# Optimization experiments

Measured on AMD Instinct MI355X. Metric: run time of the kernel, lower is better.

Reference implementation:

```python
import jax, jax.numpy as jnp
import numpy as np

N, E = 50000, 800000
IN, HID, HEADS, LAT = 128, 64, 4, 32
NEG_SLOPE = 0.2  # PyG GATv2Conv default negative_slope


def _glorot(key, shape):
    fan_in, fan_out = shape[0], shape[-1]
    lim = (6.0 / (fan_in + fan_out)) ** 0.5
    return jax.random.uniform(key, shape, jnp.float32, -lim, lim)


def setup_inputs() -> dict:
    keys = jax.random.split(jax.random.key(0), 10)
    x = jax.random.normal(keys[0], (N, IN), jnp.float32)
    edge_index = jax.random.randint(keys[1], (2, E), 0, N, jnp.int32)
    return {
        "x": x,
        "edge_index": edge_index,
        # layer 1: in -> hidden, heads=HEADS, concat=True
        "W_l1": _glorot(keys[2], (IN, HEADS * HID)),
        "W_r1": _glorot(keys[3], (IN, HEADS * HID)),
        "att1": _glorot(keys[4], (HEADS, HID)),
        "bias1": jnp.zeros((HEADS * HID,), jnp.float32),
        # layer 2: heads*hidden -> latent, heads=1, concat=False
        "W_l2": _glorot(keys[5], (HEADS * HID, LAT)),
        "W_r2": _glorot(keys[6], (HEADS * HID, LAT)),
        "att2": _glorot(keys[7], (1, LAT)),
        "bias2": jnp.zeros((LAT,), jnp.float32),
    }


def gatv2_layer(x, src, dst, W_l, W_r, att, bias, heads, out_ch, concat):
    """PyG GATv2Conv (eval mode, add_self_loops already applied to src/dst)."""
    n = x.shape[0]
    xl = (x @ W_l).reshape(n, heads, out_ch)  # source transform (messages)
    xr = (x @ W_r).reshape(n, heads, out_ch)  # target transform
    # per-edge attention logits: a^T LeakyReLU(xl[j] + xr[i])
    e = jax.nn.leaky_relu(xl[src] + xr[dst], NEG_SLOPE)  # [E, H, C]
    score = jnp.einsum('ehc,hc->eh', e, att)             # [E, H]
    # segment softmax over incoming edges of each dst node
    smax = jax.ops.segment_max(score, dst, num_segments=n)   # [N, H]
    ex = jnp.exp(score - smax[dst])
    denom = jax.ops.segment_sum(ex, dst, num_segments=n)     # [N, H]
    alpha = ex / denom[dst]                                  # [E, H]
    # scatter-add weighted source features
    out = jax.ops.segment_sum(xl[src] * alpha[..., None], dst, num_segments=n)
    out = out.reshape(n, heads * out_ch) if concat else out.mean(axis=1)
    return out + bias


def reference(x, edge_index, W_l1, W_r1, att1, bias1, W_l2, W_r2, att2, bias2):
    n = x.shape[0]
    # GATv2Conv adds self loops by default
    loops = jnp.arange(n, dtype=edge_index.dtype)
    src = jnp.concatenate([edge_index[0], loops])
    dst = jnp.concatenate([edge_index[1], loops])
    h = jax.nn.elu(gatv2_layer(x, src, dst, W_l1, W_r1, att1, bias1, HEADS, HID, True))
    z = gatv2_layer(h, src, dst, W_l2, W_r2, att2, bias2, 1, LAT, False)
    # decode: sigmoid(<z[row], z[col]>) over the original edges
    row, col = edge_index[0], edge_index[1]
    pred = jax.nn.sigmoid(jnp.sum(z[row] * z[col], axis=1))
    return pred
```

## Files before the change

kernel.cpp:

```cpp
#include <hip/hip_runtime.h>
#include <hip/hip_fp16.h>
#include <math.h>

#define N_NODES 50000
#define N_EDGES 800000
#define EP (N_EDGES + N_NODES)
#define IN_CH 128
#define HID 64
#define HEADS 4
#define F1 (HEADS * HID)
#define LAT 32
#define NEG 0.2f
#define CAP 64
#define NW (512 * 128 + 64 * 256)
#define ZQ 412502

typedef __attribute__((ext_vector_type(8))) short short8;
typedef __attribute__((ext_vector_type(8))) unsigned short ushort8v;
typedef __attribute__((ext_vector_type(4))) float f32x4;
typedef __attribute__((ext_vector_type(4))) unsigned int uint4v;

__device__ __forceinline__ unsigned short f2bf(float f) {
    unsigned int x = __float_as_uint(f);
    x += 0x7fffu + ((x >> 16) & 1u);
    return (unsigned short)(x >> 16);
}
__device__ __forceinline__ float bf2f(unsigned short u) {
    return __uint_as_float(((unsigned int)u) << 16);
}
__device__ __forceinline__ float h2f(unsigned short u) {
    return __half2float(__ushort_as_half(u));
}
__device__ __forceinline__ f32x4 mfma_bf16(short8 a, short8 b, f32x4 c) {
    return __builtin_amdgcn_mfma_f32_16x16x32_bf16(a, b, c, 0, 0, 0);
}
__device__ __forceinline__ unsigned cvt_pk_bf16(float lo, float hi) {
    unsigned r;
    asm("v_cvt_pk_bf16_f32 %0, %1, %2" : "=v"(r) : "v"(lo), "v"(hi));
    return r;
}
__device__ __forceinline__ short8 pack_bf16x8(float4 A, float4 B) {
    uint4v u;
    u[0] = cvt_pk_bf16(A.x, A.y);
    u[1] = cvt_pk_bf16(A.z, A.w);
    u[2] = cvt_pk_bf16(B.x, B.y);
    u[3] = cvt_pk_bf16(B.z, B.w);
    return __builtin_bit_cast(short8, u);
}

__global__ void conv_w_zero(const float* __restrict__ Wl1, const float* __restrict__ Wr1,
                            const float* __restrict__ Wl2, const float* __restrict__ Wr2,
                            unsigned short* __restrict__ Wt1, unsigned short* __restrict__ Wt2,
                            int4* __restrict__ zbase) {
    int idx = blockIdx.x * 256 + threadIdx.x;
    if (idx < ZQ) zbase[idx] = make_int4(0, 0, 0, 0);
    if (idx < 512 * 128) {
        int n = idx >> 7, k = idx & 127;
        float v = (n < 256) ? Wl1[(size_t)k * 256 + n] : Wr1[(size_t)k * 256 + (n - 256)];
        Wt1[idx] = f2bf(v);
    } else if (idx < NW) {
        int j = idx - 512 * 128;
        int n = j >> 8, k = j & 255;
        float v = (n < 32) ? Wl2[(size_t)k * 32 + n] : Wr2[(size_t)k * 32 + (n - 32)];
        Wt2[j] = f2bf(v);
    }
}

__global__ __launch_bounds__(256) void gemm1_mfma(const float* __restrict__ x,
                                                  const unsigned short* __restrict__ Wt1,
                                                  unsigned short* __restrict__ xlh,
                                                  unsigned short* __restrict__ xrh) {
    int wave = threadIdx.x >> 6;
    int lane = threadIdx.x & 63;
    int quad = lane >> 4, lo = lane & 15;
    int row0 = blockIdx.x * 32;
    int colw = wave * 128;
    int rB0 = min(row0 + lo, N_NODES - 1);
    int rB1 = min(row0 + 16 + lo, N_NODES - 1);
    f32x4 acc[2][8];
#pragma unroll
    for (int rt = 0; rt < 2; rt++)
#pragma unroll
        for (int ct = 0; ct < 8; ct++) acc[rt][ct] = (f32x4){0.f, 0.f, 0.f, 0.f};
#pragma unroll
    for (int ks = 0; ks < 4; ks++) {
        int koff = ks * 32 + quad * 8;
        float4 fa0 = *(const float4*)(x + (size_t)rB0 * IN_CH + koff);
        float4 fb0 = *(const float4*)(x + (size_t)rB0 * IN_CH + koff + 4);
        float4 fa1 = *(const float4*)(x + (size_t)rB1 * IN_CH + koff);
        float4 fb1 = *(const float4*)(x + (size_t)rB1 * IN_CH + koff + 4);
        short8 b0 = pack_bf16x8(fa0, fb0);
        short8 b1 = pack_bf16x8(fa1, fb1);
#pragma unroll
        for (int ct = 0; ct < 8; ct++) {
            short8 a = *(const short8*)(Wt1 + (size_t)(colw + ct * 16 + lo) * IN_CH + koff);
            acc[0][ct] = mfma_bf16(a, b0, acc[0][ct]);
            acc[1][ct] = mfma_bf16(a, b1, acc[1][ct]);
        }
    }
#pragma unroll
    for (int rt = 0; rt < 2; rt++) {
        int node = row0 + rt * 16 + lo;
        if (node < N_NODES) {
#pragma unroll
            for (int ct = 0; ct < 8; ct++) {
                int feat = colw + ct * 16 + quad * 4;
                uint2 u;
                u.x = cvt_pk_bf16(acc[rt][ct][0], acc[rt][ct][1]);
                u.y = cvt_pk_bf16(acc[rt][ct][2], acc[rt][ct][3]);
                if (feat < F1)
                    *(uint2*)(xlh + (size_t)node * F1 + feat) = u;
                else
                    *(uint2*)(xrh + (size_t)node * F1 + (feat - F1)) = u;
            }
        }
    }
}

__global__ void scatter_bucket(const int* __restrict__ ei, int* __restrict__ cnt,
                               unsigned short* __restrict__ srcsP) {
    long e = (long)blockIdx.x * 256 + threadIdx.x;
    if (e >= EP) return;
    int s, d;
    if (e < N_EDGES) { s = ei[e]; d = ei[N_EDGES + e]; }
    else             { s = d = (int)(e - N_EDGES); }
    int pos = atomicAdd(&cnt[d], 1);
    if (pos < CAP) __builtin_nontemporal_store((unsigned short)s, &srcsP[(d << 6) + pos]);
}

__global__ __launch_bounds__(256) void fused_l1(const unsigned short* __restrict__ xlh,
                                                const unsigned short* __restrict__ xrh,
                                                unsigned short* __restrict__ hbf,
                                                const unsigned short* __restrict__ srcsP,
                                                const int* __restrict__ cnt,
                                                const float* __restrict__ att,
                                                const float* __restrict__ bias,
                                                int d0) {
    int wave = threadIdx.x >> 6;
    int lane = threadIdx.x & 63;
    int h = lane >> 5;
    int c = lane & 31;
    int c0 = c << 3;
    int d = d0 + blockIdx.x * 4 + wave;
    if (d >= N_NODES) return;
    ushort8v xru = *(const ushort8v*)(xrh + (size_t)d * F1 + c0);
    float4 atA = *(const float4*)(att + c0);
    float4 atB = *(const float4*)(att + c0 + 4);
    float xr8[8], at8[8] = {atA.x, atA.y, atA.z, atA.w, atB.x, atB.y, atB.z, atB.w};
    float a6[8], a4[8];
#pragma unroll
    for (int i = 0; i < 8; i++) {
        xr8[i] = bf2f(xru[i]);
        a6[i] = 0.6f * at8[i];
        a4[i] = 0.4f * at8[i];
    }
    int start = d << 6;
    int dg    = min(CAP, __builtin_amdgcn_readfirstlane(cnt[d]));
    float l = 0.f;
    float acc[8] = {};
    int jj = h;
    int s = srcsP[start + jj];
    ushort8v raw = *(const ushort8v*)(xlh + (size_t)s * F1 + c0);
    int sN = srcsP[start + jj + 2];
    int iters = (dg + 1) >> 1;
    for (int k = 0; k < iters; k++) {
        ushort8v cr = raw;
        raw = *(const ushort8v*)(xlh + (size_t)sN * F1 + c0);
        sN = srcsP[start + jj + 4];
        float a[8];
#pragma unroll
        for (int i = 0; i < 8; i++) a[i] = bf2f(cr[i]);
        float sc = 0.f;
#pragma unroll
        for (int i = 0; i < 8; i++) {
            float v = a[i] + xr8[i];
            sc = fmaf(v, a6[i], sc);
            sc = fmaf(fabsf(v), a4[i], sc);
        }
        sc += __shfl_xor(sc, 1);
        sc += __shfl_xor(sc, 2);
        sc += __shfl_xor(sc, 4);
        float ex = (jj < dg) ? __expf(sc) : 0.f;
        l += ex;
#pragma unroll
        for (int i = 0; i < 8; i++) acc[i] = fmaf(ex, a[i], acc[i]);
        jj += 2;
    }
    l += __shfl_xor(l, 32);
#pragma unroll
    for (int i = 0; i < 8; i++) acc[i] += __shfl_xor(acc[i], 32);
    if (h == 0) {
        float inv = 1.0f / l;
        float4 bA = *(const float4*)(bias + c0);
        float4 bB = *(const float4*)(bias + c0 + 4);
        float b8[8] = {bA.x, bA.y, bA.z, bA.w, bB.x, bB.y, bB.z, bB.w};
        ushort8v ho;
#pragma unroll
        for (int i = 0; i < 8; i++) {
            float o = acc[i] * inv + b8[i];
            o = o > 0.f ? o : __expf(o) - 1.0f;
            ho[i] = (unsigned short)f2bf(o);
        }
        *(ushort8v*)(hbf + (size_t)d * F1 + c0) = ho;
    }
}

__global__ __launch_bounds__(256) void gemm2_mfma(const unsigned short* __restrict__ hbf,
                                                  const unsigned short* __restrict__ Wt2,
                                                  __half* __restrict__ xl2h,
                                                  float* __restrict__ xr2) {
    int wave = threadIdx.x >> 6;
    int lane = threadIdx.x & 63;
    int quad = lane >> 4, lo = lane & 15;
    int row0 = blockIdx.x * 64 + wave * 16;
    int rB = min(row0 + lo, N_NODES - 1);
    f32x4 acc[4];
#pragma unroll
    for (int ct = 0; ct < 4; ct++) acc[ct] = (f32x4){0.f, 0.f, 0.f, 0.f};
#pragma unroll
    for (int ks = 0; ks < 8; ks++) {
        int koff = ks * 32 + quad * 8;
        short8 b = *(const short8*)(hbf + (size_t)rB * F1 + koff);
#pragma unroll
        for (int ct = 0; ct < 4; ct++) {
            short8 a = *(const short8*)(Wt2 + (size_t)(ct * 16 + lo) * F1 + koff);
            acc[ct] = mfma_bf16(a, b, acc[ct]);
        }
    }
    int node = row0 + lo;
    if (node < N_NODES) {
#pragma unroll
        for (int ct = 0; ct < 4; ct++) {
            int feat = ct * 16 + quad * 4;
            if (feat < LAT) {
                ushort4 u;
                u.x = __half_as_ushort(__float2half_rn(acc[ct][0]));
                u.y = __half_as_ushort(__float2half_rn(acc[ct][1]));
                u.z = __half_as_ushort(__float2half_rn(acc[ct][2]));
                u.w = __half_as_ushort(__float2half_rn(acc[ct][3]));
                *(ushort4*)((unsigned short*)xl2h + (size_t)node * LAT + feat) = u;
            } else {
                float4 f = make_float4(acc[ct][0], acc[ct][1], acc[ct][2], acc[ct][3]);
                *(float4*)(xr2 + (size_t)node * LAT + (feat - LAT)) = f;
            }
        }
    }
}

__global__ __launch_bounds__(256) void fused_l2(const __half* __restrict__ xl2h,
                                                const float* __restrict__ xr2,
                                                const unsigned short* __restrict__ srcsP,
                                                const int* __restrict__ cnt,
                                                const float* __restrict__ att,
                                                const float* __restrict__ bias,
                                                __half* __restrict__ zh) {
    int wave = threadIdx.x >> 6;
    int lane = threadIdx.x & 63;
    int q = lane >> 4;
    int c = lane & 15;
    int c2 = c << 1;
    int d = blockIdx.x * 4 + wave;
    if (d >= N_NODES) return;
    float xr0 = xr2[(size_t)d * LAT + c2];
    float xr1v = xr2[(size_t)d * LAT + c2 + 1];
    float av0 = att[c2], av1 = att[c2 + 1];
    float a60 = 0.6f * av0, a40 = 0.4f * av0;
    float a61 = 0.6f * av1, a41 = 0.4f * av1;
    int start = d << 6;
    int dg    = min(CAP, __builtin_amdgcn_readfirstlane(cnt[d]));
    float l = 0.f, acc0 = 0.f, acc1 = 0.f;
    int jj = q;
    int s = srcsP[start + jj];
    __half2 raw = *(const __half2*)(xl2h + (size_t)s * LAT + c2);
    int sN = srcsP[start + jj + 4];
    int iters = (dg + 3) >> 2;
    for (int k = 0; k < iters; k++) {
        __half2 cr = raw;
        raw = *(const __half2*)(xl2h + (size_t)sN * LAT + c2);
        sN = srcsP[start + jj + 8];
        float a0 = __half2float(cr.x), a1 = __half2float(cr.y);
        float v0 = a0 + xr0;
        float v1 = a1 + xr1v;
        float sc = 0.f;
        sc = fmaf(v0, a60, sc);
        sc = fmaf(fabsf(v0), a40, sc);
        sc = fmaf(v1, a61, sc);
        sc = fmaf(fabsf(v1), a41, sc);
        sc += __shfl_xor(sc, 1);
        sc += __shfl_xor(sc, 2);
        sc += __shfl_xor(sc, 4);
        sc += __shfl_xor(sc, 8);
        float ex = (jj < dg) ? __expf(sc) : 0.f;
        l += ex;
        acc0 = fmaf(ex, a0, acc0);
        acc1 = fmaf(ex, a1, acc1);
        jj += 4;
    }
    l += __shfl_xor(l, 16); acc0 += __shfl_xor(acc0, 16); acc1 += __shfl_xor(acc1, 16);
    l += __shfl_xor(l, 32); acc0 += __shfl_xor(acc0, 32); acc1 += __shfl_xor(acc1, 32);
    if (q == 0) {
        __half2 o;
        o.x = __float2half_rn(acc0 / l + bias[c2]);
        o.y = __float2half_rn(acc1 / l + bias[c2 + 1]);
        *(__half2*)(zh + (size_t)d * LAT + c2) = o;
    }
}

__global__ __launch_bounds__(256) void decode(const __half* __restrict__ zh,
                                              const int* __restrict__ ei,
                                              float* __restrict__ out) {
    int g = threadIdx.x >> 2;
    int lane = threadIdx.x & 3;
    long e = (long)blockIdx.x * 64 + g;
    if (e >= N_EDGES) return;
    int r = ei[e], c = ei[N_EDGES + e];
    int cc = lane << 3;
    ushort8v ur = *(const ushort8v*)((const unsigned short*)zh + (size_t)r * LAT + cc);
    ushort8v uc = *(const ushort8v*)((const unsigned short*)zh + (size_t)c * LAT + cc);
    float v = 0.f;
#pragma unroll
    for (int i = 0; i < 8; i++) {
        v += h2f(ur[i]) * h2f(uc[i]);
    }
    v += __shfl_xor(v, 1);
    v += __shfl_xor(v, 2);
    if (lane == 0) out[e] = 1.0f / (1.0f + __expf(-v));
}

extern "C" void kernel_launch(void* const* d_in, const int* in_sizes, int n_in,
                              void* d_out, int out_size, void* d_ws, size_t ws_size,
                              hipStream_t stream) {
    const float* x    = (const float*)d_in[0];
    const int*   ei   = (const int*)d_in[1];
    const float* Wl1  = (const float*)d_in[2];
    const float* Wr1  = (const float*)d_in[3];
    const float* att1 = (const float*)d_in[4];
    const float* b1   = (const float*)d_in[5];
    const float* Wl2  = (const float*)d_in[6];
    const float* Wr2  = (const float*)d_in[7];
    const float* att2 = (const float*)d_in[8];
    const float* b2   = (const float*)d_in[9];
    float* out = (float*)d_out;

    unsigned short* xrh = (unsigned short*)d_ws;
    unsigned short* hbf = xrh + (size_t)N_NODES * F1;
    unsigned short* xlh = hbf + (size_t)N_NODES * F1;
    int* cnt = (int*)(xlh + (size_t)N_NODES * F1);
    unsigned short* srcsP = (unsigned short*)(cnt + N_NODES);
    unsigned short* Wt1 = srcsP + (size_t)N_NODES * CAP + 16;
    unsigned short* Wt2 = Wt1 + 512 * 128;
    __half* xl2h = (__half*)xlh;
    float*  xr2  = (float*)(xl2h + (size_t)N_NODES * LAT);
    __half* zh   = (__half*)(xr2 + (size_t)N_NODES * LAT);

    conv_w_zero<<<(ZQ + 255) / 256, 256, 0, stream>>>(Wl1, Wr1, Wl2, Wr2, Wt1, Wt2,
                                                      (int4*)cnt);

    scatter_bucket<<<(EP + 255) / 256, 256, 0, stream>>>(ei, cnt, srcsP);

    gemm1_mfma<<<(N_NODES + 31) / 32, 256, 0, stream>>>(x, Wt1, xlh, xrh);

    fused_l1<<<25000 / 4, 256, 0, stream>>>(xlh, xrh, hbf, srcsP, cnt, att1, b1, 0);
    fused_l1<<<25000 / 4, 256, 0, stream>>>(xlh, xrh, hbf, srcsP, cnt, att1, b1, 25000);

    gemm2_mfma<<<(N_NODES + 63) / 64, 256, 0, stream>>>(hbf, Wt2, xl2h, xr2);
    fused_l2<<<(N_NODES + 3) / 4, 256, 0, stream>>>(xl2h, xr2, srcsP, cnt, att2, b2, zh);

    decode<<<(N_EDGES + 63) / 64, 256, 0, stream>>>(zh, ei, out);
}
```

Baseline: 332.2 us.

## Merge edge bucketing and first GEMM into one launch; single fused_l1 launch

Combines the scatter_bucket kernel and the layer-1 GEMM into one grid, interleaving scatter blocks and GEMM blocks so the atomic-bound scatter and the MFMA-bound GEMM run concurrently. It also collapses the two half-sized fused_l1 launches into one. This removes launch gaps and idle tail time between independent stages. The cost is a larger register footprint for the combined kernel, which is sized for the GEMM path and may lower occupancy for the scatter blocks.

```diff
diff --git a/kernel.cpp b/kernel.cpp
--- a/kernel.cpp
+++ b/kernel.cpp
@@ -14,6 +14,8 @@
 #define CAP 64
 #define NW (512 * 128 + 64 * 256)
 #define ZQ 412502
+#define G1B ((N_NODES + 31) / 32)
+#define SCB ((EP + 255) / 256)
 
 typedef __attribute__((ext_vector_type(8))) short short8;
 typedef __attribute__((ext_vector_type(8))) unsigned short ushort8v;
@@ -66,14 +68,35 @@
     }
 }
 
-__global__ __launch_bounds__(256) void gemm1_mfma(const float* __restrict__ x,
-                                                  const unsigned short* __restrict__ Wt1,
-                                                  unsigned short* __restrict__ xlh,
-                                                  unsigned short* __restrict__ xrh) {
+__global__ __launch_bounds__(256) void gemm1_scatter(const float* __restrict__ x,
+                                                     const unsigned short* __restrict__ Wt1,
+                                                     unsigned short* __restrict__ xlh,
+                                                     unsigned short* __restrict__ xrh,
+                                                     const int* __restrict__ ei,
+                                                     int* __restrict__ cnt,
+                                                     unsigned short* __restrict__ srcsP) {
+    int bid = blockIdx.x;
+    bool isScatter;
+    int wid;
+    if (bid < 2 * G1B) { isScatter = (bid & 1); wid = bid >> 1; }
+    else               { isScatter = true;      wid = G1B + (bid - 2 * G1B); }
+
+    if (isScatter) {
+        long e = (long)wid * 256 + threadIdx.x;
+        if (e >= EP) return;
+        int s, d;
+        if (e < N_EDGES) { s = ei[e]; d = ei[N_EDGES + e]; }
+        else             { s = d = (int)(e - N_EDGES); }
+        int pos = atomicAdd(&cnt[d], 1);
+        if (pos < CAP)
+            __builtin_nontemporal_store((unsigned short)s, &srcsP[(d << 6) + pos]);
+        return;
+    }
+
     int wave = threadIdx.x >> 6;
     int lane = threadIdx.x & 63;
     int quad = lane >> 4, lo = lane & 15;
-    int row0 = blockIdx.x * 32;
+    int row0 = wid * 32;
     int colw = wave * 128;
     int rB0 = min(row0 + lo, N_NODES - 1);
     int rB1 = min(row0 + 16 + lo, N_NODES - 1);
@@ -117,31 +140,19 @@
     }
 }
 
-__global__ void scatter_bucket(const int* __restrict__ ei, int* __restrict__ cnt,
-                               unsigned short* __restrict__ srcsP) {
-    long e = (long)blockIdx.x * 256 + threadIdx.x;
-    if (e >= EP) return;
-    int s, d;
-    if (e < N_EDGES) { s = ei[e]; d = ei[N_EDGES + e]; }
-    else             { s = d = (int)(e - N_EDGES); }
-    int pos = atomicAdd(&cnt[d], 1);
-    if (pos < CAP) __builtin_nontemporal_store((unsigned short)s, &srcsP[(d << 6) + pos]);
-}
-
 __global__ __launch_bounds__(256) void fused_l1(const unsigned short* __restrict__ xlh,
                                                 const unsigned short* __restrict__ xrh,
                                                 unsigned short* __restrict__ hbf,
                                                 const unsigned short* __restrict__ srcsP,
                                                 const int* __restrict__ cnt,
                                                 const float* __restrict__ att,
-                                                const float* __restrict__ bias,
-                                                int d0) {
+                                                const float* __restrict__ bias) {
     int wave = threadIdx.x >> 6;
     int lane = threadIdx.x & 63;
     int h = lane >> 5;
     int c = lane & 31;
     int c0 = c << 3;
-    int d = d0 + blockIdx.x * 4 + wave;
+    int d = blockIdx.x * 4 + wave;
     if (d >= N_NODES) return;
     ushort8v xru = *(const ushort8v*)(xrh + (size_t)d * F1 + c0);
     float4 atA = *(const float4*)(att + c0);
@@ -356,12 +367,10 @@
     conv_w_zero<<<(ZQ + 255) / 256, 256, 0, stream>>>(Wl1, Wr1, Wl2, Wr2, Wt1, Wt2,
                                                       (int4*)cnt);
 
-    scatter_bucket<<<(EP + 255) / 256, 256, 0, stream>>>(ei, cnt, srcsP);
-
-    gemm1_mfma<<<(N_NODES + 31) / 32, 256, 0, stream>>>(x, Wt1, xlh, xrh);
-
-    fused_l1<<<25000 / 4, 256, 0, stream>>>(xlh, xrh, hbf, srcsP, cnt, att1, b1, 0);
-    fused_l1<<<25000 / 4, 256, 0, stream>>>(xlh, xrh, hbf, srcsP, cnt, att1, b1, 25000);
+    gemm1_scatter<<<2 * G1B + (SCB - G1B), 256, 0, stream>>>(x, Wt1, xlh, xrh,
+                                                             ei, cnt, srcsP);
+
+    fused_l1<<<(N_NODES + 3) / 4, 256, 0, stream>>>(xlh, xrh, hbf, srcsP, cnt, att1, b1);
 
     gemm2_mfma<<<(N_NODES + 63) / 64, 256, 0, stream>>>(hbf, Wt2, xl2h, xr2);
     fused_l2<<<(N_NODES + 3) / 4, 256, 0, stream>>>(xl2h, xr2, srcsP, cnt, att2, b2, zh);
```

After: 311.7 us. 6.2% less time.
